# Performance work log

Measured on AMD Instinct MI355X. Metric: run time of the kernel, lower is better.

## Reference

```python
import jax, jax.numpy as jnp
import numpy as np

# MMoE: E experts, each a 2-layer relu MLP (D->H0->H1); T softmax gates over experts.

def setup_inputs() -> dict:
    B, D, H0, H1, E, T = 16384, 1024, 1024, 512, 8, 2
    key = jax.random.key(0)
    ks = jax.random.split(key, 7)
    def glorot(k, shape, fan_in, fan_out):
        lim = jnp.sqrt(6.0 / (fan_in + fan_out)).astype(jnp.float32)
        return jax.random.uniform(k, shape, jnp.float32, -lim, lim)
    inputs = jax.random.normal(ks[0], (B, D), jnp.float32)
    W0 = glorot(ks[1], (E, D, H0), D, H0)      # expert layer 0 kernels
    b0 = jnp.zeros((E, H0), jnp.float32)
    W1 = glorot(ks[2], (E, H0, H1), H0, H1)    # expert layer 1 kernels
    b1 = jnp.zeros((E, H1), jnp.float32)
    Wg = glorot(ks[3], (T, D, E), D, E)        # gate kernels per task
    bg = jnp.zeros((T, E), jnp.float32)
    return {"inputs": inputs, "W0": W0, "b0": b0, "W1": W1, "b1": b1, "Wg": Wg, "bg": bg}


def reference(inputs, W0, b0, W1, b1, Wg, bg):
    # Experts: batched GEMMs over expert axis e.  h: [E, B, H]
    h = jax.nn.relu(jnp.einsum('bd,edh->ebh', inputs, W0) + b0[:, None, :])
    expert_out = jax.nn.relu(jnp.einsum('ebh,ehk->ebk', h, W1) + b1[:, None, :])  # [E, B, H1]
    # Gates: softmax over experts per task.  g: [T, B, E]
    gates = jax.nn.softmax(jnp.einsum('bd,tde->tbe', inputs, Wg) + bg[:, None, :], axis=-1)
    # Gate-weighted sum of expert outputs (einsum 'ai,ian->an' per task)
    outs = jnp.einsum('tbe,ebk->tbk', gates, expert_out)  # [T, B, H1]
    return tuple(outs[t] for t in range(outs.shape[0]))
```

## Files before the change

### kernel.cpp

```cpp
#include <hip/hip_runtime.h>

#define Bsz 16384
#define Dd  1024
#define H0d 1024
#define H1d 512
#define Ee  8
#define Tt  2

typedef short  s8_t  __attribute__((ext_vector_type(8)));
typedef float  fx4   __attribute__((ext_vector_type(4)));
typedef __bf16 bf8_t __attribute__((ext_vector_type(8)));

__device__ __forceinline__ ushort f2bf(float f) {
    uint u = __builtin_bit_cast(uint, f);
    uint r = u + 0x7fffu + ((u >> 16) & 1u);
    return (ushort)(r >> 16);
}
__device__ __forceinline__ float bf2f(ushort u) {
    uint x = ((uint)u) << 16;
    return __builtin_bit_cast(float, x);
}
__device__ __forceinline__ void gload16(const void* g, void* l) {
    __builtin_amdgcn_global_load_lds((const __attribute__((address_space(1))) uint*)g,
                                     (__attribute__((address_space(3))) uint*)l, 16, 0, 0);
}
__device__ __forceinline__ bf8_t ldbf8(const ushort* p) {
    s8_t v = *(const s8_t*)p;
    return __builtin_bit_cast(bf8_t, v);
}

__global__ __launch_bounds__(256) void cvt_bf16_vec(const float* __restrict__ X,
                                                    ushort* __restrict__ Y, int n8) {
    int i = blockIdx.x * 256 + threadIdx.x;
    if (i >= n8) return;
    const float4* p = (const float4*)X + (size_t)i * 2;
    float4 a = p[0], b = p[1];
    s8_t o;
    o[0] = (short)f2bf(a.x); o[1] = (short)f2bf(a.y); o[2] = (short)f2bf(a.z); o[3] = (short)f2bf(a.w);
    o[4] = (short)f2bf(b.x); o[5] = (short)f2bf(b.y); o[6] = (short)f2bf(b.z); o[7] = (short)f2bf(b.w);
    ((s8_t*)Y)[i] = o;
}

__global__ __launch_bounds__(256) void transpose_cvt(const float* __restrict__ W,
                                                     ushort* __restrict__ WT, int R, int Cc) {
    __shared__ float tile[32][33];
    int e = blockIdx.z;
    int r0 = blockIdx.x * 32, c0 = blockIdx.y * 32;
    const float* Wp = W  + (size_t)e * R * Cc;
    ushort*      Tp = WT + (size_t)e * R * Cc;
    int tx = threadIdx.x, ty = threadIdx.y;
    #pragma unroll
    for (int i = 0; i < 32; i += 8)
        tile[ty + i][tx] = Wp[(size_t)(r0 + ty + i) * Cc + c0 + tx];
    __syncthreads();
    #pragma unroll
    for (int i = 0; i < 32; i += 8)
        Tp[(size_t)(c0 + ty + i) * R + r0 + tx] = f2bf(tile[tx][ty + i]);
}

__global__ __launch_bounds__(256) void transpose_wg(const float* __restrict__ Wg,
                                                    ushort* __restrict__ WgT) {
    int i = blockIdx.x * 256 + threadIdx.x;
    int d = i & 1023, r = i >> 10;
    int t = r >> 3, e = r & 7;
    WgT[i] = f2bf(Wg[((size_t)t * 1024 + d) * 8 + e]);
}

__global__ __launch_bounds__(256) void gates_mfma(const ushort* __restrict__ Xb,
                                                  const ushort* __restrict__ WgT,
                                                  const float* __restrict__ bg,
                                                  float* __restrict__ gts) {
    int wave = threadIdx.x >> 6, lane = threadIdx.x & 63;
    int base = blockIdx.x * 64 + wave * 16;
    int l15 = lane & 15, lhi = lane >> 4;
    fx4 acc0 = {}, acc1 = {};
    const ushort* xp = Xb  + (size_t)(base + l15) * Dd + lhi * 8;
    const ushort* wp = WgT + (size_t)l15 * Dd + lhi * 8;
    #pragma unroll
    for (int kt = 0; kt < 32; kt += 2) {
        bf8_t a0 = ldbf8(xp + kt * 32);
        bf8_t b0 = ldbf8(wp + kt * 32);
        bf8_t a1 = ldbf8(xp + kt * 32 + 32);
        bf8_t b1 = ldbf8(wp + kt * 32 + 32);
        acc0 = __builtin_amdgcn_mfma_f32_16x16x32_bf16(a0, b0, acc0, 0, 0, 0);
        acc1 = __builtin_amdgcn_mfma_f32_16x16x32_bf16(a1, b1, acc1, 0, 0, 0);
    }
    fx4 acc = acc0 + acc1;
    float bgv = bg[l15];
    int t = l15 >> 3, e = l15 & 7;
    #pragma unroll
    for (int r = 0; r < 4; ++r) {
        float v = acc[r] + bgv;
        float mx = v;
        mx = fmaxf(mx, __shfl_xor(mx, 1));
        mx = fmaxf(mx, __shfl_xor(mx, 2));
        mx = fmaxf(mx, __shfl_xor(mx, 4));
        float p = expf(v - mx);
        float s = p;
        s += __shfl_xor(s, 1); s += __shfl_xor(s, 2); s += __shfl_xor(s, 4);
        int row = base + lhi * 4 + r;
        gts[(size_t)t * Bsz * 8 + (size_t)row * 8 + e] = p / s;
    }
}

__global__ __launch_bounds__(1024, 4) void gemm256(
    const ushort* __restrict__ Abase, const ushort* __restrict__ BtBase,
    const float* __restrict__ biasBase, ushort* __restrict__ CBase,
    int N, int K, int nbn, size_t aStride) {
    __shared__ ushort lds[65536];
    char* ldsc = (char*)lds;

    const int tid = threadIdx.x;
    const int wave = tid >> 6, lane = tid & 63;
    const int l15 = lane & 15, lhi = lane >> 4;
    const int wr = wave >> 2, wc = wave & 3;

    const int ey = blockIdx.y;
    const ushort* A    = Abase   + (size_t)ey * aStride;
    const ushort* Bt   = BtBase  + (size_t)ey * (size_t)N * K;
    const float*  bias = biasBase + (size_t)ey * N;
    ushort*       C    = CBase   + (size_t)ey * (size_t)Bsz * N;

    int nwg = gridDim.x, wg = blockIdx.x;
    int q = nwg >> 3;
    int swz = (wg & 7) * q + (wg >> 3);
    const int bm = (swz / nbn) * 256, bn = (swz % nbn) * 256;

    const int srcslot = (lane & 7) ^ (lane >> 3);
    const ushort* aSrc = A  + (size_t)(bm + wave * 8 + (lane >> 3)) * K + srcslot * 8;
    const ushort* bSrc = Bt + (size_t)(bn + wave * 8 + (lane >> 3)) * K + srcslot * 8;
    const int sc0 = lhi ^ (l15 & 7);
    const int sc1 = (4 | lhi) ^ (l15 & 7);

    fx4 acc[4][4] = {};

    const int nK = K >> 6;

#define STAGE(KT, d)                                                                            \
    {                                                                                           \
        gload16(aSrc + (size_t)(KT)*64,                ldsc + ((d)*32768 + wave * 1024));       \
        gload16(aSrc + (size_t)128 * K + (size_t)(KT)*64,                                       \
                ldsc + ((d)*32768 + 16384 + wave * 1024));                                      \
        gload16(bSrc + (size_t)(KT)*64,                ldsc + (65536 + (d)*32768 + wave * 1024));\
        gload16(bSrc + (size_t)128 * K + (size_t)(KT)*64,                                       \
                ldsc + (65536 + (d)*32768 + 16384 + wave * 1024));                              \
    }

    STAGE(0, 0);
    __syncthreads();

    for (int kt = 0; kt < nK; ++kt) {
        const int cur = kt & 1;
        if (kt + 1 < nK) STAGE(kt + 1, cur ^ 1);
        bf8_t aF[4][2], bF[4][2];
        #pragma unroll
        for (int m = 0; m < 4; ++m) {
            int Rb = cur * 32768 + (wr * 64 + m * 16 + l15) * 128;
            aF[m][0] = ldbf8((const ushort*)(ldsc + Rb + sc0 * 16));
            aF[m][1] = ldbf8((const ushort*)(ldsc + Rb + sc1 * 16));
        }
        #pragma unroll
        for (int n = 0; n < 4; ++n) {
            int Rb = 65536 + cur * 32768 + (wc * 64 + n * 16 + l15) * 128;
            bF[n][0] = ldbf8((const ushort*)(ldsc + Rb + sc0 * 16));
            bF[n][1] = ldbf8((const ushort*)(ldsc + Rb + sc1 * 16));
        }
        #pragma unroll
        for (int m = 0; m < 4; ++m)
            #pragma unroll
            for (int n = 0; n < 4; ++n)
                #pragma unroll
                for (int kk = 0; kk < 2; ++kk)
                    acc[m][n] = __builtin_amdgcn_mfma_f32_16x16x32_bf16(
                        aF[m][kk], bF[n][kk], acc[m][n], 0, 0, 0);
        __syncthreads();
    }
#undef STAGE

    float bv[4];
    #pragma unroll
    for (int ni = 0; ni < 4; ++ni) bv[ni] = bias[bn + wc * 64 + ni * 16 + l15];
    #pragma unroll
    for (int mi = 0; mi < 4; ++mi) {
        #pragma unroll
        for (int rr = 0; rr < 4; ++rr) {
            int row = bm + wr * 64 + mi * 16 + lhi * 4 + rr;
            ushort* cp = C + (size_t)row * N + bn + wc * 64 + l15;
            #pragma unroll
            for (int ni = 0; ni < 4; ++ni) {
                float v = acc[mi][ni][rr] + bv[ni];
                v = fmaxf(v, 0.f);
                cp[ni * 16] = f2bf(v);
            }
        }
    }
}

__global__ __launch_bounds__(1024, 4) void gemm256x128(
    const ushort* __restrict__ Abase, const ushort* __restrict__ BtBase,
    const float* __restrict__ biasBase, ushort* __restrict__ CBase,
    int N, int K, int nbn, size_t aStride) {
    __shared__ ushort lds[49152];
    char* ldsc = (char*)lds;

    const int tid = threadIdx.x;
    const int wave = tid >> 6, lane = tid & 63;
    const int l15 = lane & 15, lhi = lane >> 4;
    const int wr = wave >> 2, wc = wave & 3;

    const int ey = blockIdx.y;
    const ushort* A    = Abase   + (size_t)ey * aStride;
    const ushort* Bt   = BtBase  + (size_t)ey * (size_t)N * K;
    const float*  bias = biasBase + (size_t)ey * N;
    ushort*       C    = CBase   + (size_t)ey * (size_t)Bsz * N;

    int nwg = gridDim.x, wg = blockIdx.x;
    int q = nwg >> 3;
    int swz = (wg & 7) * q + (wg >> 3);
    const int bm = (swz / nbn) * 256, bn = (swz % nbn) * 128;

    const int srcslot = (lane & 7) ^ (lane >> 3);
    const ushort* aSrc = A  + (size_t)(bm + wave * 8 + (lane >> 3)) * K + srcslot * 8;
    const ushort* bSrc = Bt + (size_t)(bn + wave * 8 + (lane >> 3)) * K + srcslot * 8;
    const int sc0 = lhi ^ (l15 & 7);
    const int sc1 = (4 | lhi) ^ (l15 & 7);

    fx4 acc[4][2] = {};

    const int nK = K >> 6;

#define STAGE(KT, d)                                                                            \
    {                                                                                           \
        gload16(aSrc + (size_t)(KT)*64,                ldsc + ((d)*32768 + wave * 1024));       \
        gload16(aSrc + (size_t)128 * K + (size_t)(KT)*64,                                       \
                ldsc + ((d)*32768 + 16384 + wave * 1024));                                      \
        gload16(bSrc + (size_t)(KT)*64,                ldsc + (65536 + (d)*16384 + wave * 1024));\
    }

    STAGE(0, 0);
    __syncthreads();

    for (int kt = 0; kt < nK; ++kt) {
        const int cur = kt & 1;
        if (kt + 1 < nK) STAGE(kt + 1, cur ^ 1);
        bf8_t aF[4][2], bF[2][2];
        #pragma unroll
        for (int m = 0; m < 4; ++m) {
            int Rb = cur * 32768 + (wr * 64 + m * 16 + l15) * 128;
            aF[m][0] = ldbf8((const ushort*)(ldsc + Rb + sc0 * 16));
            aF[m][1] = ldbf8((const ushort*)(ldsc + Rb + sc1 * 16));
        }
        #pragma unroll
        for (int n = 0; n < 2; ++n) {
            int Rb = 65536 + cur * 16384 + (wc * 32 + n * 16 + l15) * 128;
            bF[n][0] = ldbf8((const ushort*)(ldsc + Rb + sc0 * 16));
            bF[n][1] = ldbf8((const ushort*)(ldsc + Rb + sc1 * 16));
        }
        #pragma unroll
        for (int m = 0; m < 4; ++m)
            #pragma unroll
            for (int n = 0; n < 2; ++n)
                #pragma unroll
                for (int kk = 0; kk < 2; ++kk)
                    acc[m][n] = __builtin_amdgcn_mfma_f32_16x16x32_bf16(
                        aF[m][kk], bF[n][kk], acc[m][n], 0, 0, 0);
        __syncthreads();
    }
#undef STAGE

    float bv[2];
    #pragma unroll
    for (int ni = 0; ni < 2; ++ni) bv[ni] = bias[bn + wc * 32 + ni * 16 + l15];
    #pragma unroll
    for (int mi = 0; mi < 4; ++mi) {
        #pragma unroll
        for (int rr = 0; rr < 4; ++rr) {
            int row = bm + wr * 64 + mi * 16 + lhi * 4 + rr;
            ushort* cp = C + (size_t)row * N + bn + wc * 32 + l15;
            #pragma unroll
            for (int ni = 0; ni < 2; ++ni) {
                float v = acc[mi][ni][rr] + bv[ni];
                v = fmaxf(v, 0.f);
                cp[ni * 16] = f2bf(v);
            }
        }
    }
}

template <int MODE>
__global__ __launch_bounds__(256, 2) void gemm_bt(
    const ushort* __restrict__ A, const ushort* __restrict__ Bt,
    const float* __restrict__ bias, ushort* __restrict__ C,
    float* __restrict__ outAcc, const float* __restrict__ gts,
    int expert, int N, int K, int nbn) {
    __shared__ ushort Ash[128 * 64];
    __shared__ ushort Bsh[128 * 64];
    const int tid = threadIdx.x;
    const int wave = tid >> 6, lane = tid & 63;

    int nwg = gridDim.x, wg = blockIdx.x;
    int q = nwg >> 3;
    int swz = (wg & 7) * q + (wg >> 3);
    const int bm = (swz / nbn) * 128, bn = (swz % nbn) * 128;

    const int wm = (wave >> 1) * 64, wn = (wave & 1) * 64;
    const int l15 = lane & 15, lhi = lane >> 4;

    fx4 acc[4][4] = {};

    const int nK = K >> 6;
    for (int kt = 0; kt < nK; ++kt) {
        __syncthreads();
        #pragma unroll
        for (int i = 0; i < 4; ++i) {
            int c = (wave * 4 + i) * 64 + lane;
            int row = c >> 3, g = c & 7;
            const ushort* ga = A + (size_t)(bm + row) * K + kt * 64 + g * 8;
            gload16(ga, (char*)Ash + (wave * 4 + i) * 1024);
            const ushort* gb = Bt + (size_t)(bn + row) * K + kt * 64 + g * 8;
            gload16(gb, (char*)Bsh + (wave * 4 + i) * 1024);
        }
        __syncthreads();
        #pragma unroll
        for (int kk = 0; kk < 2; ++kk) {
            bf8_t af[4], bf_[4];
            #pragma unroll
            for (int m = 0; m < 4; ++m)
                af[m] = ldbf8((const ushort*)((const char*)Ash + (wm + m * 16 + l15) * 128 + kk * 64 + lhi * 16));
            #pragma unroll
            for (int n = 0; n < 4; ++n)
                bf_[n] = ldbf8((const ushort*)((const char*)Bsh + (wn + n * 16 + l15) * 128 + kk * 64 + lhi * 16));
            #pragma unroll
            for (int m = 0; m < 4; ++m)
                #pragma unroll
                for (int n = 0; n < 4; ++n)
                    acc[m][n] = __builtin_amdgcn_mfma_f32_16x16x32_bf16(af[m], bf_[n], acc[m][n], 0, 0, 0);
        }
    }

    #pragma unroll
    for (int m = 0; m < 4; ++m) {
        #pragma unroll
        for (int r = 0; r < 4; ++r) {
            int row = bm + wm + m * 16 + lhi * 4 + r;
            if (MODE == 0) {
                ushort* cp = C + (size_t)row * N + bn + wn + l15;
                #pragma unroll
                for (int n = 0; n < 4; ++n) {
                    float v = acc[m][n][r] + bias[bn + wn + n * 16 + l15];
                    v = fmaxf(v, 0.f);
                    cp[n * 16] = f2bf(v);
                }
            } else {
                float g0 = gts[(size_t)row * 8 + expert];
                float g1 = gts[(size_t)Bsz * 8 + (size_t)row * 8 + expert];
                #pragma unroll
                for (int n = 0; n < 4; ++n) {
                    int col = bn + wn + n * 16 + l15;
                    float v = acc[m][n][r] + bias[col];
                    v = fmaxf(v, 0.f);
                    float* o0 = outAcc + (size_t)row * N + col;
                    float* o1 = outAcc + (size_t)Bsz * N + (size_t)row * N + col;
                    *o0 += g0 * v;
                    *o1 += g1 * v;
                }
            }
        }
    }
}

__global__ __launch_bounds__(256) void combine_kernel(const ushort* __restrict__ eo,
                                                      const float* __restrict__ gts,
                                                      float* __restrict__ out) {
    int wave = threadIdx.x >> 6, lane = threadIdx.x & 63;
    int b = blockIdx.x * 4 + wave;
    float g0[8], g1[8];
    #pragma unroll
    for (int e = 0; e < 8; ++e) {
        g0[e] = gts[(size_t)b * 8 + e];
        g1[e] = gts[(size_t)Bsz * 8 + (size_t)b * 8 + e];
    }
    int k0 = lane * 8;
    float a0[8], a1[8];
    #pragma unroll
    for (int j = 0; j < 8; ++j) { a0[j] = 0.f; a1[j] = 0.f; }
    #pragma unroll
    for (int e = 0; e < 8; ++e) {
        s8_t v = *(const s8_t*)(eo + ((size_t)e * Bsz + b) * H1d + k0);
        #pragma unroll
        for (int j = 0; j < 8; ++j) {
            float f = bf2f((ushort)v[j]);
            a0[j] += g0[e] * f;
            a1[j] += g1[e] * f;
        }
    }
    float4* o0 = (float4*)(out + (size_t)b * H1d + k0);
    o0[0] = make_float4(a0[0], a0[1], a0[2], a0[3]);
    o0[1] = make_float4(a0[4], a0[5], a0[6], a0[7]);
    float4* o1 = (float4*)(out + (size_t)Bsz * H1d + (size_t)b * H1d + k0);
    o1[0] = make_float4(a1[0], a1[1], a1[2], a1[3]);
    o1[1] = make_float4(a1[4], a1[5], a1[6], a1[7]);
}

extern "C" void kernel_launch(void* const* d_in, const int* in_sizes, int n_in,
                              void* d_out, int out_size, void* d_ws, size_t ws_size,
                              hipStream_t stream) {
    const float* X  = (const float*)d_in[0];
    const float* W0 = (const float*)d_in[1];
    const float* b0 = (const float*)d_in[2];
    const float* W1 = (const float*)d_in[3];
    const float* b1 = (const float*)d_in[4];
    const float* Wg = (const float*)d_in[5];
    const float* bg = (const float*)d_in[6];
    float* out = (float*)d_out;

    size_t off = 0;
    auto alloc = [&](size_t bytes) {
        char* p = (char*)d_ws + off;
        off += (bytes + 255) & ~(size_t)255;
        return (void*)p;
    };
    ushort* Xb  = (ushort*)alloc((size_t)Bsz * Dd * 2);
    ushort* W0T = (ushort*)alloc((size_t)Ee * Dd * H0d * 2);
    ushort* W1T = (ushort*)alloc((size_t)Ee * H0d * H1d * 2);
    float*  gts = (float*)alloc((size_t)Tt * Bsz * Ee * 4);
    ushort* WgT = (ushort*)alloc((size_t)Tt * Ee * Dd * 2);
    size_t eoBytes = (size_t)Ee * Bsz * H1d * 2;
    size_t hBytes  = (size_t)Bsz * H0d * 2;
    bool use_eo = (off + eoBytes + hBytes + 512) <= ws_size;
    ushort* eo = use_eo ? (ushort*)alloc(eoBytes) : nullptr;
    int EB = 1;
    if (use_eo) {
        size_t rem = (ws_size > off) ? ws_size - off : 0;
        if (rem >= 8 * (hBytes + 256)) EB = 8;
        else if (rem >= 4 * (hBytes + 256)) EB = 4;
        else if (rem >= 2 * (hBytes + 256)) EB = 2;
    }
    ushort* hG = (ushort*)alloc((size_t)EB * hBytes);

    cvt_bf16_vec<<<(Bsz * Dd / 8 + 255) / 256, 256, 0, stream>>>(X, Xb, Bsz * Dd / 8);
    transpose_cvt<<<dim3(Dd / 32, H0d / 32, Ee), dim3(32, 8), 0, stream>>>(W0, W0T, Dd, H0d);
    transpose_cvt<<<dim3(H0d / 32, H1d / 32, Ee), dim3(32, 8), 0, stream>>>(W1, W1T, H0d, H1d);
    transpose_wg<<<(Tt * Ee * Dd) / 256, 256, 0, stream>>>(Wg, WgT);
    gates_mfma<<<Bsz / 64, 256, 0, stream>>>(Xb, WgT, bg, gts);
    if (!use_eo) hipMemsetAsync(d_out, 0, (size_t)out_size * sizeof(float), stream);

    if (use_eo) {
        for (int g = 0; g < Ee; g += EB) {
            gemm256<<<dim3((Bsz / 256) * (H0d / 256), EB), 1024, 0, stream>>>(
                Xb, W0T + (size_t)g * Dd * H0d, b0 + (size_t)g * H0d, hG,
                H0d, Dd, H0d / 256, 0);
            gemm256x128<<<dim3((Bsz / 256) * (H1d / 128), EB), 1024, 0, stream>>>(
                hG, W1T + (size_t)g * H0d * H1d, b1 + (size_t)g * H1d,
                eo + (size_t)g * Bsz * H1d, H1d, H0d, H1d / 128, (size_t)Bsz * H0d);
        }
        combine_kernel<<<Bsz / 4, 256, 0, stream>>>(eo, gts, out);
    } else {
        for (int e = 0; e < Ee; ++e) {
            gemm256<<<dim3((Bsz / 256) * (H0d / 256), 1), 1024, 0, stream>>>(
                Xb, W0T + (size_t)e * Dd * H0d, b0 + (size_t)e * H0d, hG,
                H0d, Dd, H0d / 256, 0);
            gemm_bt<1><<<dim3((Bsz / 128) * (H1d / 128)), 256, 0, stream>>>(
                hG, W1T + (size_t)e * H0d * H1d, b1 + (size_t)e * H1d,
                nullptr, out, gts, e, H1d, H0d, H1d / 128);
        }
    }
}
```

Measured before the change: 508.1 us.

## Chunk batch into 4096-row slices processing all experts per chunk

Restructures the expert pipeline to iterate over batch chunks of 4096 rows, running all 8 experts per launch for layer 0, layer 1, and the gate-weighted combine. Intermediates (h for all experts, expert outputs) are sized per chunk, which shrinks the workspace footprint so the intermediates can stay more cache-resident between stages. In exchange there are more kernel launches, and each GEMM grid is smaller per chunk (but multiplied by 8 experts).

Result: slower. 528.8 us (+4.1%).

```diff
diff --git a/kernel.cpp b/kernel.cpp
--- a/kernel.cpp
+++ b/kernel.cpp
@@ -6,6 +6,7 @@
 #define H1d 512
 #define Ee  8
 #define Tt  2
+#define CH  4096
 
 typedef short  s8_t  __attribute__((ext_vector_type(8)));
 typedef float  fx4   __attribute__((ext_vector_type(4)));
@@ -106,7 +107,7 @@
 __global__ __launch_bounds__(1024, 4) void gemm256(
     const ushort* __restrict__ Abase, const ushort* __restrict__ BtBase,
     const float* __restrict__ biasBase, ushort* __restrict__ CBase,
-    int N, int K, int nbn, size_t aStride) {
+    int N, int K, int nbn, size_t aStride, int mrows) {
     __shared__ ushort lds[65536];
     char* ldsc = (char*)lds;
 
@@ -119,7 +120,7 @@
     const ushort* A    = Abase   + (size_t)ey * aStride;
     const ushort* Bt   = BtBase  + (size_t)ey * (size_t)N * K;
     const float*  bias = biasBase + (size_t)ey * N;
-    ushort*       C    = CBase   + (size_t)ey * (size_t)Bsz * N;
+    ushort*       C    = CBase   + (size_t)ey * (size_t)mrows * N;
 
     int nwg = gridDim.x, wg = blockIdx.x;
     int q = nwg >> 3;
@@ -199,7 +200,7 @@
 __global__ __launch_bounds__(1024, 4) void gemm256x128(
     const ushort* __restrict__ Abase, const ushort* __restrict__ BtBase,
     const float* __restrict__ biasBase, ushort* __restrict__ CBase,
-    int N, int K, int nbn, size_t aStride) {
+    int N, int K, int nbn, size_t aStride, int mrows) {
     __shared__ ushort lds[49152];
     char* ldsc = (char*)lds;
 
@@ -212,7 +213,7 @@
     const ushort* A    = Abase   + (size_t)ey * aStride;
     const ushort* Bt   = BtBase  + (size_t)ey * (size_t)N * K;
     const float*  bias = biasBase + (size_t)ey * N;
-    ushort*       C    = CBase   + (size_t)ey * (size_t)Bsz * N;
+    ushort*       C    = CBase   + (size_t)ey * (size_t)mrows * N;
 
     int nwg = gridDim.x, wg = blockIdx.x;
     int q = nwg >> 3;
@@ -371,14 +372,16 @@
 
 __global__ __launch_bounds__(256) void combine_kernel(const ushort* __restrict__ eo,
                                                       const float* __restrict__ gts,
-                                                      float* __restrict__ out) {
+                                                      float* __restrict__ out,
+                                                      int chunkBase) {
     int wave = threadIdx.x >> 6, lane = threadIdx.x & 63;
     int b = blockIdx.x * 4 + wave;
+    int gb = chunkBase + b;
     float g0[8], g1[8];
     #pragma unroll
     for (int e = 0; e < 8; ++e) {
-        g0[e] = gts[(size_t)b * 8 + e];
-        g1[e] = gts[(size_t)Bsz * 8 + (size_t)b * 8 + e];
+        g0[e] = gts[(size_t)gb * 8 + e];
+        g1[e] = gts[(size_t)Bsz * 8 + (size_t)gb * 8 + e];
     }
     int k0 = lane * 8;
     float a0[8], a1[8];
@@ -386,7 +389,7 @@
     for (int j = 0; j < 8; ++j) { a0[j] = 0.f; a1[j] = 0.f; }
     #pragma unroll
     for (int e = 0; e < 8; ++e) {
-        s8_t v = *(const s8_t*)(eo + ((size_t)e * Bsz + b) * H1d + k0);
+        s8_t v = *(const s8_t*)(eo + ((size_t)e * CH + b) * H1d + k0);
         #pragma unroll
         for (int j = 0; j < 8; ++j) {
             float f = bf2f((ushort)v[j]);
@@ -394,10 +397,10 @@
             a1[j] += g1[e] * f;
         }
     }
-    float4* o0 = (float4*)(out + (size_t)b * H1d + k0);
+    float4* o0 = (float4*)(out + (size_t)gb * H1d + k0);
     o0[0] = make_float4(a0[0], a0[1], a0[2], a0[3]);
     o0[1] = make_float4(a0[4], a0[5], a0[6], a0[7]);
-    float4* o1 = (float4*)(out + (size_t)Bsz * H1d + (size_t)b * H1d + k0);
+    float4* o1 = (float4*)(out + (size_t)Bsz * H1d + (size_t)gb * H1d + k0);
     o1[0] = make_float4(a1[0], a1[1], a1[2], a1[3]);
     o1[1] = make_float4(a1[4], a1[5], a1[6], a1[7]);
 }
@@ -425,43 +428,37 @@
     ushort* W1T = (ushort*)alloc((size_t)Ee * H0d * H1d * 2);
     float*  gts = (float*)alloc((size_t)Tt * Bsz * Ee * 4);
     ushort* WgT = (ushort*)alloc((size_t)Tt * Ee * Dd * 2);
-    size_t eoBytes = (size_t)Ee * Bsz * H1d * 2;
-    size_t hBytes  = (size_t)Bsz * H0d * 2;
-    bool use_eo = (off + eoBytes + hBytes + 512) <= ws_size;
-    ushort* eo = use_eo ? (ushort*)alloc(eoBytes) : nullptr;
-    int EB = 1;
-    if (use_eo) {
-        size_t rem = (ws_size > off) ? ws_size - off : 0;
-        if (rem >= 8 * (hBytes + 256)) EB = 8;
-        else if (rem >= 4 * (hBytes + 256)) EB = 4;
-        else if (rem >= 2 * (hBytes + 256)) EB = 2;
-    }
-    ushort* hG = (ushort*)alloc((size_t)EB * hBytes);
+
+    size_t h8Bytes = (size_t)Ee * CH * H0d * 2;
+    size_t eoBytes = (size_t)Ee * CH * H1d * 2;
+    bool chunked = (off + h8Bytes + eoBytes + 512) <= ws_size;
 
     cvt_bf16_vec<<<(Bsz * Dd / 8 + 255) / 256, 256, 0, stream>>>(X, Xb, Bsz * Dd / 8);
     transpose_cvt<<<dim3(Dd / 32, H0d / 32, Ee), dim3(32, 8), 0, stream>>>(W0, W0T, Dd, H0d);
     transpose_cvt<<<dim3(H0d / 32, H1d / 32, Ee), dim3(32, 8), 0, stream>>>(W1, W1T, H0d, H1d);
     transpose_wg<<<(Tt * Ee * Dd) / 256, 256, 0, stream>>>(Wg, WgT);
     gates_mfma<<<Bsz / 64, 256, 0, stream>>>(Xb, WgT, bg, gts);
-    if (!use_eo) hipMemsetAsync(d_out, 0, (size_t)out_size * sizeof(float), stream);
-
-    if (use_eo) {
-        for (int g = 0; g < Ee; g += EB) {
-            gemm256<<<dim3((Bsz / 256) * (H0d / 256), EB), 1024, 0, stream>>>(
-                Xb, W0T + (size_t)g * Dd * H0d, b0 + (size_t)g * H0d, hG,
-                H0d, Dd, H0d / 256, 0);
-            gemm256x128<<<dim3((Bsz / 256) * (H1d / 128), EB), 1024, 0, stream>>>(
-                hG, W1T + (size_t)g * H0d * H1d, b1 + (size_t)g * H1d,
-                eo + (size_t)g * Bsz * H1d, H1d, H0d, H1d / 128, (size_t)Bsz * H0d);
-        }
-        combine_kernel<<<Bsz / 4, 256, 0, stream>>>(eo, gts, out);
+
+    if (chunked) {
+        ushort* h8 = (ushort*)alloc(h8Bytes);
+        ushort* eo = (ushort*)alloc(eoBytes);
+        for (int c = 0; c < Bsz / CH; ++c) {
+            const ushort* Xc = Xb + (size_t)c * CH * Dd;
+            gemm256<<<dim3((CH / 256) * (H0d / 256), Ee), 1024, 0, stream>>>(
+                Xc, W0T, b0, h8, H0d, Dd, H0d / 256, 0, CH);
+            gemm256x128<<<dim3((CH / 256) * (H1d / 128), Ee), 1024, 0, stream>>>(
+                h8, W1T, b1, eo, H1d, H0d, H1d / 128, (size_t)CH * H0d, CH);
+            combine_kernel<<<CH / 4, 256, 0, stream>>>(eo, gts, out, c * CH);
+        }
     } else {
+        ushort* h1 = (ushort*)alloc((size_t)CH * H0d * 2 * (Bsz / CH));
+        hipMemsetAsync(d_out, 0, (size_t)out_size * sizeof(float), stream);
         for (int e = 0; e < Ee; ++e) {
             gemm256<<<dim3((Bsz / 256) * (H0d / 256), 1), 1024, 0, stream>>>(
-                Xb, W0T + (size_t)e * Dd * H0d, b0 + (size_t)e * H0d, hG,
-                H0d, Dd, H0d / 256, 0);
+                Xb, W0T + (size_t)e * Dd * H0d, b0 + (size_t)e * H0d, h1,
+                H0d, Dd, H0d / 256, 0, Bsz);
             gemm_bt<1><<<dim3((Bsz / 128) * (H1d / 128)), 256, 0, stream>>>(
-                hG, W1T + (size_t)e * H0d * H1d, b1 + (size_t)e * H1d,
+                h1, W1T + (size_t)e * H0d * H1d, b1 + (size_t)e * H1d,
                 nullptr, out, gts, e, H1d, H0d, H1d / 128);
         }
     }
```
